# Kernel optimization log

Measured on AMD Instinct MI355X. Metric: run time of the kernel, lower is better.

The kernel has to match this reference:

```python
import math
import jax, jax.numpy as jnp
import numpy as np

H = 16
D_MODEL = 1024
D_K = D_MODEL // H


def setup_inputs() -> dict:
    key = jax.random.key(0)
    ks = jax.random.split(key, 12)
    B, S = 4, 2048
    scale = 1.0 / math.sqrt(D_MODEL)
    inp = {
        "query": jax.random.normal(ks[0], (B, S, D_MODEL), jnp.float32),
        "key": jax.random.normal(ks[1], (B, S, D_MODEL), jnp.float32),
        "value": jax.random.normal(ks[2], (B, S, D_MODEL), jnp.float32),
        "mask": jnp.ones((B, 1, 1, S), jnp.int32),
        "Wq": jax.random.normal(ks[3], (D_MODEL, D_MODEL), jnp.float32) * scale,
        "bq": jnp.zeros((D_MODEL,), jnp.float32),
        "Wk": jax.random.normal(ks[4], (D_MODEL, D_MODEL), jnp.float32) * scale,
        "bk": jnp.zeros((D_MODEL,), jnp.float32),
        "Wv": jax.random.normal(ks[5], (D_MODEL, D_MODEL), jnp.float32) * scale,
        "bv": jnp.zeros((D_MODEL,), jnp.float32),
        "Wo": jax.random.normal(ks[6], (D_MODEL, D_MODEL), jnp.float32) * scale,
        "bo": jnp.zeros((D_MODEL,), jnp.float32),
    }
    return inp


def _split_heads(x, W, b):
    # x: (B, S, d_model) -> (B, H, S, d_k); torch Linear: x @ W.T + b
    B, S, _ = x.shape
    y = x @ W.T + b
    return y.reshape(B, S, H, D_K).transpose(0, 2, 1, 3)


def reference(query, key, value, mask, Wq, bq, Wk, bk, Wv, bv, Wo, bo):
    B, Sq, _ = query.shape
    q = _split_heads(query, Wq, bq)   # (B,H,Sq,dk)
    k = _split_heads(key, Wk, bk)     # (B,H,Skv,dk)
    v = _split_heads(value, Wv, bv)   # (B,H,Skv,dk)
    scores = jnp.einsum('bhqd,bhkd->bhqk', q, k) / math.sqrt(D_K)
    scores = jnp.where(mask == 0, jnp.float32(-1e9), scores)
    p_attn = jax.nn.softmax(scores, axis=-1)  # dropout p=0 (eval)
    x = jnp.einsum('bhqk,bhkd->bhqd', p_attn, v)
    x = x.transpose(0, 2, 1, 3).reshape(B, Sq, H * D_K)
    return x @ Wo.T + bo
```

## Files before the change

### kernel.cpp

```cpp
#include <hip/hip_runtime.h>
#include <hip/hip_bf16.h>
#include <stdint.h>

typedef unsigned short u16;
typedef short bf16x8 __attribute__((ext_vector_type(8)));
typedef float f32x4 __attribute__((ext_vector_type(4)));

#define D_MODEL 1024
#define NHEAD 16
#define DK 64
#define SEQ 2048
#define NB 4
#define MTOT (NB * SEQ)

__device__ __forceinline__ u16 f2bf(float f) {
  union { float f; unsigned u; } x; x.f = f;
  unsigned r = x.u + 0x7FFFu + ((x.u >> 16) & 1u);
  return (u16)(r >> 16);
}
#if __has_builtin(__builtin_amdgcn_cvt_pk_bf16_f32)
__device__ __forceinline__ unsigned pkbf(float a, float b) {
  auto r = __builtin_amdgcn_cvt_pk_bf16_f32(a, b);
  union { decltype(r) v; unsigned u; } c; c.v = r; return c.u;
}
#else
__device__ __forceinline__ unsigned pkbf(float a, float b) {
  return (unsigned)f2bf(a) | ((unsigned)f2bf(b) << 16);
}
#endif
#if __has_builtin(__builtin_amdgcn_exp2f)
__device__ __forceinline__ float exp2r(float x) { return __builtin_amdgcn_exp2f(x); }
#else
__device__ __forceinline__ float exp2r(float x) { return exp2f(x); }
#endif
__device__ __forceinline__ void gl_lds16(const u16* g, u16* s) {
  __builtin_amdgcn_global_load_lds(
      (const __attribute__((address_space(1))) void*)g,
      (__attribute__((address_space(3))) void*)s, 16, 0, 0);
}

__global__ __launch_bounds__(256) void cvt1(const float4* __restrict__ src,
                                            uint2* __restrict__ dst, int n4) {
  for (int i = blockIdx.x * 256 + threadIdx.x; i < n4; i += gridDim.x * 256) {
    float4 x = src[i];
    uint2 o;
    o.x = pkbf(x.x, x.y);
    o.y = pkbf(x.z, x.w);
    dst[i] = o;
  }
}
__global__ __launch_bounds__(256) void cvt4(const float4* __restrict__ s0,
                                            const float4* __restrict__ s1,
                                            const float4* __restrict__ s2,
                                            const float4* __restrict__ s3,
                                            uint2* __restrict__ dst, int n4each) {
  const float4* s = (blockIdx.y == 0) ? s0 : (blockIdx.y == 1) ? s1
                  : (blockIdx.y == 2) ? s2 : s3;
  uint2* d = dst + (size_t)blockIdx.y * n4each;
  for (int i = blockIdx.x * 256 + threadIdx.x; i < n4each; i += gridDim.x * 256) {
    float4 x = s[i];
    uint2 o;
    o.x = pkbf(x.x, x.y);
    o.y = pkbf(x.z, x.w);
    d[i] = o;
  }
}

template <int MODE>
__global__ __launch_bounds__(256, 4) void gemm_bt64(
    const u16* __restrict__ A, const u16* __restrict__ W,
    const float* __restrict__ bias, void* __restrict__ out, float scale)
{
  __shared__ alignas(16) u16 smem[12288];
  u16* As = smem;
  u16* Bs = smem + 4096;

  const int tid = threadIdx.x;
  const int l = tid & 63, w = tid >> 6;
  const int lq = l & 15, qd = l >> 4;
  const int wm = (w >> 1) << 5, wn = (w & 1) << 6;
  const int m0 = blockIdx.y << 6, n0 = blockIdx.x << 7;

  int arow[2], ak8[2], brow[4], bk8[4];
#pragma unroll
  for (int r = 0; r < 2; ++r) {
    int c = r * 256 + tid;
    arow[r] = c >> 3; ak8[r] = (c & 7) ^ (arow[r] & 7);
  }
#pragma unroll
  for (int r = 0; r < 4; ++r) {
    int c = r * 256 + tid;
    brow[r] = c >> 3; bk8[r] = (c & 7) ^ (brow[r] & 7);
  }
  int aoff[2][2], boff[4][2];
#pragma unroll
  for (int i = 0; i < 2; ++i) {
    int mr = wm + (i << 4) + lq;
#pragma unroll
    for (int s = 0; s < 2; ++s)
      aoff[i][s] = (mr << 6) + ((((s << 2) + qd) ^ (mr & 7)) << 3);
  }
#pragma unroll
  for (int j = 0; j < 4; ++j) {
    int nr = wn + (j << 4) + lq;
#pragma unroll
    for (int s = 0; s < 2; ++s)
      boff[j][s] = (nr << 6) + ((((s << 2) + qd) ^ (nr & 7)) << 3);
  }

  const u16* Ab = A + (size_t)m0 * D_MODEL;
  const u16* Bb = W + (size_t)n0 * D_MODEL;

  f32x4 acc[2][4] = {};

  for (int kt = 0; kt < 16; ++kt) {
    const int kbase = kt << 6;
#pragma unroll
    for (int r = 0; r < 2; ++r)
      gl_lds16(Ab + (size_t)arow[r] * D_MODEL + kbase + (ak8[r] << 3), As + ((r * 256 + tid) << 3));
#pragma unroll
    for (int r = 0; r < 4; ++r)
      gl_lds16(Bb + (size_t)brow[r] * D_MODEL + kbase + (bk8[r] << 3), Bs + ((r * 256 + tid) << 3));
    __syncthreads();
#pragma unroll
    for (int s = 0; s < 2; ++s) {
      bf16x8 af[2], bfv[4];
#pragma unroll
      for (int i = 0; i < 2; ++i) af[i] = *(const bf16x8*)(As + aoff[i][s]);
#pragma unroll
      for (int j = 0; j < 4; ++j) bfv[j] = *(const bf16x8*)(Bs + boff[j][s]);
#pragma unroll
      for (int i = 0; i < 2; ++i)
#pragma unroll
        for (int j = 0; j < 4; ++j)
          acc[i][j] = __builtin_amdgcn_mfma_f32_16x16x32_bf16(af[i], bfv[j], acc[i][j], 0, 0, 0);
    }
    __syncthreads();
  }

  if (MODE == 1) {
    u16* Cs = smem;
    u16* outb = (u16*)out;
#pragma unroll
    for (int i = 0; i < 2; ++i)
#pragma unroll
      for (int j = 0; j < 4; ++j) {
        int ml = wm + (i << 4) + (qd << 2);
        int nl = wn + (j << 4) + lq;
        float bj = bias[n0 + nl];
        uint2 pk;
        pk.x = pkbf(acc[i][j][0] + bj, acc[i][j][1] + bj);
        pk.y = pkbf(acc[i][j][2] + bj, acc[i][j][3] + bj);
        *(uint2*)(Cs + nl * 80 + ml) = pk;
      }
    __syncthreads();
    int nl = tid >> 1, sh = (tid & 1) << 5;
    int n = n0 + nl;
    int b_ = m0 >> 11;
    const uint4* src = (const uint4*)(Cs + nl * 80 + sh);
    uint4* dst = (uint4*)(outb +
        (((size_t)b_ * NHEAD + (n >> 6)) * DK + (n & 63)) * SEQ + (m0 & 2047) + sh);
#pragma unroll
    for (int e = 0; e < 4; ++e) dst[e] = src[e];
  } else {
    u16* outb = (u16*)out;
    float* outf = (float*)out;
#pragma unroll
    for (int i = 0; i < 2; ++i)
#pragma unroll
      for (int j = 0; j < 4; ++j) {
        int ml = m0 + wm + (i << 4) + (qd << 2);
        int n = n0 + wn + (j << 4) + lq;
        float bj = bias[n];
#pragma unroll
        for (int r = 0; r < 4; ++r) {
          int m = ml + r;
          float v = (acc[i][j][r] + bj) * scale;
          if (MODE == 0)
            outb[(((size_t)(m >> 11) * NHEAD + (n >> 6)) * SEQ + (m & 2047)) * DK + (n & 63)] = f2bf(v);
          else
            outf[(size_t)m * D_MODEL + n] = v;
        }
      }
  }
}

__global__ __launch_bounds__(256, 4) void attn_fused(
    const u16* __restrict__ Q,
    const u16* __restrict__ K,
    const u16* __restrict__ Vt,
    const int* __restrict__ mask,
    u16* __restrict__ X)
{
  __shared__ alignas(16) u16 PQ[8192];
  __shared__ alignas(16) u16 Ks[4096];
  __shared__ alignas(16) u16 Vs[5120];
  __shared__ alignas(16) float mbf[64];

  const int tid = threadIdx.x;
  const int l = tid & 63, w = tid >> 6;
  const int lq = l & 15, qd = l >> 4;
  const int bh = blockIdx.y;
  const int q0 = blockIdx.x << 7;
  const int b_ = bh >> 4, h = bh & 15;
  const size_t base = (size_t)bh * SEQ * DK;
  const int wq0 = w << 5;

#pragma unroll
  for (int r = 0; r < 4; ++r) {
    int c = r * 256 + tid;
    int row = c >> 3, k8 = (c & 7) ^ (row & 7);
    gl_lds16(Q + base + (size_t)(q0 + row) * DK + (k8 << 3), PQ + (c << 3));
  }
  {
    unsigned v = (tid < 16) ? 0x3F803F80u : 0u;
    uint2 pk; pk.x = v; pk.y = v;
    *(uint2*)(Vs + 4096 + tid * 4) = pk;
  }
  __syncthreads();

  bf16x8 qf[2][2];
#pragma unroll
  for (int i = 0; i < 2; ++i)
#pragma unroll
    for (int s = 0; s < 2; ++s) {
      int row = wq0 + (i << 4) + lq;
      qf[i][s] = *(const bf16x8*)(PQ + (row << 6) + ((((s << 2) + qd) ^ (row & 7)) << 3));
    }

  f32x4 Ov[2][4] = {};
  f32x4 Ovl[2] = {};

  for (int t = 0; t < 32; ++t) {
    const int kv0 = t << 6;
    __syncthreads();
#pragma unroll
    for (int r = 0; r < 2; ++r) {
      int c = r * 256 + tid;
      int row = c >> 3, k8 = (c & 7) ^ (row & 7);
      gl_lds16(K + base + (size_t)(kv0 + row) * DK + (k8 << 3), Ks + (c << 3));
    }
#pragma unroll
    for (int r = 0; r < 2; ++r) {
      int c = r * 256 + tid;
      int row = c >> 3, k8 = (c & 7) ^ (row & 7);
      gl_lds16(Vt + base + (size_t)row * SEQ + kv0 + (k8 << 3), Vs + (c << 3));
    }
    if (tid < 64)
      mbf[tid] = mask[b_ * SEQ + kv0 + tid] ? 0.0f : -1.44269504e9f;
    __syncthreads();

    float4 m4[4];
#pragma unroll
    for (int jb = 0; jb < 4; ++jb) m4[jb] = *(const float4*)(mbf + (jb << 4) + (qd << 2));

    f32x4 Sc[4][2];
#pragma unroll
    for (int jb = 0; jb < 4; ++jb)
#pragma unroll
      for (int i = 0; i < 2; ++i) {
        Sc[jb][i][0] = m4[jb].x; Sc[jb][i][1] = m4[jb].y;
        Sc[jb][i][2] = m4[jb].z; Sc[jb][i][3] = m4[jb].w;
      }
#pragma unroll
    for (int s = 0; s < 2; ++s) {
      bf16x8 kf[4];
#pragma unroll
      for (int jb = 0; jb < 4; ++jb) {
        int row = (jb << 4) + lq;
        kf[jb] = *(const bf16x8*)(Ks + (row << 6) + ((((s << 2) + qd) ^ (row & 7)) << 3));
      }
#pragma unroll
      for (int jb = 0; jb < 4; ++jb)
#pragma unroll
        for (int i = 0; i < 2; ++i)
          Sc[jb][i] = __builtin_amdgcn_mfma_f32_16x16x32_bf16(kf[jb], qf[i][s], Sc[jb][i], 0, 0, 0);
    }

#pragma unroll
    for (int i = 0; i < 2; ++i) {
      const int prow = wq0 + (i << 4) + lq;
      const int rbase = prow << 6;
      const int rsw = prow & 7;
#pragma unroll
      for (int jb = 0; jb < 4; ++jb) {
        float p0 = exp2r(Sc[jb][i][0]);
        float p1 = exp2r(Sc[jb][i][1]);
        float p2 = exp2r(Sc[jb][i][2]);
        float p3 = exp2r(Sc[jb][i][3]);
        uint2 pk;
        pk.x = pkbf(p0, p1);
        pk.y = pkbf(p2, p3);
        int c = (jb << 1) + (qd >> 1);
        *(uint2*)(PQ + rbase + ((c ^ rsw) << 3) + ((qd & 1) << 2)) = pk;
      }
    }

#pragma unroll
    for (int s = 0; s < 2; ++s) {
      bf16x8 pf[2], vf[4], vf1;
#pragma unroll
      for (int i = 0; i < 2; ++i) {
        int prow = wq0 + (i << 4) + lq;
        pf[i] = *(const bf16x8*)(PQ + (prow << 6) + ((((s << 2) + qd) ^ (prow & 7)) << 3));
      }
#pragma unroll
      for (int j = 0; j < 4; ++j) {
        int row = (j << 4) + lq;
        vf[j] = *(const bf16x8*)(Vs + (row << 6) + ((((s << 2) + qd) ^ (row & 7)) << 3));
      }
      {
        int row = 64 + lq;
        vf1 = *(const bf16x8*)(Vs + (row << 6) + ((((s << 2) + qd) ^ (row & 7)) << 3));
      }
#pragma unroll
      for (int i = 0; i < 2; ++i) {
#pragma unroll
        for (int j = 0; j < 4; ++j)
          Ov[i][j] = __builtin_amdgcn_mfma_f32_16x16x32_bf16(pf[i], vf[j], Ov[i][j], 0, 0, 0);
        Ovl[i] = __builtin_amdgcn_mfma_f32_16x16x32_bf16(pf[i], vf1, Ovl[i], 0, 0, 0);
      }
    }
  }

#pragma unroll
  for (int i = 0; i < 2; ++i) {
    float inv[4];
#pragma unroll
    for (int r = 0; r < 4; ++r) inv[r] = 1.0f / Ovl[i][r];
#pragma unroll
    for (int r = 0; r < 4; ++r) {
      float sc_ = __shfl(inv[r], l & 48);
      int qrow = q0 + wq0 + (i << 4) + (qd << 2) + r;
#pragma unroll
      for (int j = 0; j < 4; ++j)
        X[((size_t)b_ * SEQ + qrow) * D_MODEL + (h << 6) + (j << 4) + lq] =
            f2bf(Ov[i][j][r] * sc_);
    }
  }
}

extern "C" void kernel_launch(void* const* d_in, const int* in_sizes, int n_in,
                              void* d_out, int out_size, void* d_ws, size_t ws_size,
                              hipStream_t stream) {
  const float* query = (const float*)d_in[0];
  const float* key_  = (const float*)d_in[1];
  const float* value = (const float*)d_in[2];
  const int* mask    = (const int*)d_in[3];
  const float* Wq = (const float*)d_in[4];
  const float* bq = (const float*)d_in[5];
  const float* Wk = (const float*)d_in[6];
  const float* bk = (const float*)d_in[7];
  const float* Wv = (const float*)d_in[8];
  const float* bv = (const float*)d_in[9];
  const float* Wo = (const float*)d_in[10];
  const float* bo = (const float*)d_in[11];

  u16* ws16 = (u16*)d_ws;
  const size_t WSZ = (size_t)D_MODEL * D_MODEL;
  const size_t ASZ = (size_t)MTOT * D_MODEL;
  u16* wqc = ws16;
  u16* wkc = ws16 + WSZ;
  u16* wvc = ws16 + 2 * WSZ;
  u16* woc = ws16 + 3 * WSZ;
  u16* C1  = ws16 + 4 * WSZ;
  u16* Qb  = ws16 + 4 * WSZ + ASZ;
  u16* Kb  = ws16 + 4 * WSZ + 2 * ASZ;
  u16* Xb  = C1;
  u16* Vtb = (u16*)d_out;

  const float SCQ = 0.125f * 1.44269504088896f;

  dim3 blk(256);
  dim3 gg(D_MODEL / 128, MTOT / 64);

  cvt4<<<dim3(256, 4), blk, 0, stream>>>((const float4*)Wq, (const float4*)Wk,
                                         (const float4*)Wv, (const float4*)Wo,
                                         (uint2*)wqc, (int)(WSZ / 4));
  cvt1<<<1024, blk, 0, stream>>>((const float4*)query, (uint2*)C1, (int)(ASZ / 4));
  gemm_bt64<0><<<gg, blk, 0, stream>>>(C1, wqc, bq, Qb, SCQ);
  cvt1<<<1024, blk, 0, stream>>>((const float4*)key_, (uint2*)C1, (int)(ASZ / 4));
  gemm_bt64<0><<<gg, blk, 0, stream>>>(C1, wkc, bk, Kb, 1.0f);
  cvt1<<<1024, blk, 0, stream>>>((const float4*)value, (uint2*)C1, (int)(ASZ / 4));
  gemm_bt64<1><<<gg, blk, 0, stream>>>(C1, wvc, bv, Vtb, 1.0f);
  attn_fused<<<dim3(SEQ / 128, NB * NHEAD), blk, 0, stream>>>(Qb, Kb, Vtb, mask, Xb);
  gemm_bt64<2><<<gg, blk, 0, stream>>>(Xb, woc, bo, d_out, 1.0f);
}
```

Measured before the change: 363.7 us.

## Batch all fp32-to-bf16 conversions and QKV projections into single launches

Result: faster. 349.6 us (-3.9%).

```diff
diff --git a/kernel.cpp b/kernel.cpp
--- a/kernel.cpp
+++ b/kernel.cpp
@@ -39,6 +39,24 @@
       (__attribute__((address_space(3))) void*)s, 16, 0, 0);
 }
 
+struct CvtArgs {
+  const float4* s[7];
+  uint2* d[7];
+  int n4[7];
+};
+__global__ __launch_bounds__(256) void cvt_all(CvtArgs a) {
+  const int y = blockIdx.y;
+  const float4* s = a.s[y];
+  uint2* d = a.d[y];
+  const int n4 = a.n4[y];
+  for (int i = blockIdx.x * 256 + threadIdx.x; i < n4; i += gridDim.x * 256) {
+    float4 x = s[i];
+    uint2 o;
+    o.x = pkbf(x.x, x.y);
+    o.y = pkbf(x.z, x.w);
+    d[i] = o;
+  }
+}
 __global__ __launch_bounds__(256) void cvt1(const float4* __restrict__ src,
                                             uint2* __restrict__ dst, int n4) {
   for (int i = blockIdx.x * 256 + threadIdx.x; i < n4; i += gridDim.x * 256) {
@@ -67,11 +85,11 @@
 }
 
 template <int MODE>
-__global__ __launch_bounds__(256, 4) void gemm_bt64(
+__device__ __forceinline__ void gemm_body(
     const u16* __restrict__ A, const u16* __restrict__ W,
-    const float* __restrict__ bias, void* __restrict__ out, float scale)
+    const float* __restrict__ bias, void* __restrict__ out, float scale,
+    int m0, int n0, u16* smem)
 {
-  __shared__ alignas(16) u16 smem[12288];
   u16* As = smem;
   u16* Bs = smem + 4096;
 
@@ -79,7 +97,6 @@
   const int l = tid & 63, w = tid >> 6;
   const int lq = l & 15, qd = l >> 4;
   const int wm = (w >> 1) << 5, wn = (w & 1) << 6;
-  const int m0 = blockIdx.y << 6, n0 = blockIdx.x << 7;
 
   int arow[2], ak8[2], brow[4], bk8[4];
 #pragma unroll
@@ -183,6 +200,33 @@
         }
       }
   }
+}
+
+template <int MODE>
+__global__ __launch_bounds__(256, 4) void gemm_bt64(
+    const u16* __restrict__ A, const u16* __restrict__ W,
+    const float* __restrict__ bias, void* __restrict__ out, float scale)
+{
+  __shared__ alignas(16) u16 smem[12288];
+  gemm_body<MODE>(A, W, bias, out, scale,
+                  blockIdx.y << 6, blockIdx.x << 7, smem);
+}
+
+__global__ __launch_bounds__(256, 4) void proj_qkv(
+    const u16* __restrict__ Cq, const u16* __restrict__ Ck, const u16* __restrict__ Cv,
+    const u16* __restrict__ wq, const u16* __restrict__ wk, const u16* __restrict__ wv,
+    const float* __restrict__ bq, const float* __restrict__ bk, const float* __restrict__ bv,
+    u16* __restrict__ Qb, u16* __restrict__ Kb, u16* __restrict__ Vt, float scq)
+{
+  __shared__ alignas(16) u16 smem[12288];
+  const int z = blockIdx.z;
+  const int m0 = blockIdx.y << 6, n0 = blockIdx.x << 7;
+  if (z == 0)
+    gemm_body<0>(Cq, wq, bq, Qb, scq, m0, n0, smem);
+  else if (z == 1)
+    gemm_body<0>(Ck, wk, bk, Kb, 1.0f, m0, n0, smem);
+  else
+    gemm_body<1>(Cv, wv, bv, Vt, 1.0f, m0, n0, smem);
 }
 
 __global__ __launch_bounds__(256, 4) void attn_fused(
@@ -359,30 +403,59 @@
   u16* ws16 = (u16*)d_ws;
   const size_t WSZ = (size_t)D_MODEL * D_MODEL;
   const size_t ASZ = (size_t)MTOT * D_MODEL;
-  u16* wqc = ws16;
-  u16* wkc = ws16 + WSZ;
-  u16* wvc = ws16 + 2 * WSZ;
-  u16* woc = ws16 + 3 * WSZ;
-  u16* C1  = ws16 + 4 * WSZ;
-  u16* Qb  = ws16 + 4 * WSZ + ASZ;
-  u16* Kb  = ws16 + 4 * WSZ + 2 * ASZ;
-  u16* Xb  = C1;
-  u16* Vtb = (u16*)d_out;
-
   const float SCQ = 0.125f * 1.44269504088896f;
 
   dim3 blk(256);
   dim3 gg(D_MODEL / 128, MTOT / 64);
 
-  cvt4<<<dim3(256, 4), blk, 0, stream>>>((const float4*)Wq, (const float4*)Wk,
-                                         (const float4*)Wv, (const float4*)Wo,
-                                         (uint2*)wqc, (int)(WSZ / 4));
-  cvt1<<<1024, blk, 0, stream>>>((const float4*)query, (uint2*)C1, (int)(ASZ / 4));
-  gemm_bt64<0><<<gg, blk, 0, stream>>>(C1, wqc, bq, Qb, SCQ);
-  cvt1<<<1024, blk, 0, stream>>>((const float4*)key_, (uint2*)C1, (int)(ASZ / 4));
-  gemm_bt64<0><<<gg, blk, 0, stream>>>(C1, wkc, bk, Kb, 1.0f);
-  cvt1<<<1024, blk, 0, stream>>>((const float4*)value, (uint2*)C1, (int)(ASZ / 4));
-  gemm_bt64<1><<<gg, blk, 0, stream>>>(C1, wvc, bv, Vtb, 1.0f);
-  attn_fused<<<dim3(SEQ / 128, NB * NHEAD), blk, 0, stream>>>(Qb, Kb, Vtb, mask, Xb);
-  gemm_bt64<2><<<gg, blk, 0, stream>>>(Xb, woc, bo, d_out, 1.0f);
-}
+  if (ws_size >= (size_t)(4 * WSZ + 4 * ASZ) * 2) {
+    u16* wqc = ws16;
+    u16* wkc = ws16 + WSZ;
+    u16* wvc = ws16 + 2 * WSZ;
+    u16* woc = ws16 + 3 * WSZ;
+    u16* Cq  = ws16 + 4 * WSZ;
+    u16* Ck  = ws16 + 4 * WSZ + ASZ;
+    u16* Qb  = ws16 + 4 * WSZ + 2 * ASZ;
+    u16* Kb  = ws16 + 4 * WSZ + 3 * ASZ;
+    u16* Xb  = Cq;
+    u16* Vtb = (u16*)d_out;
+    u16* Cv  = (u16*)d_out + ASZ;
+
+    CvtArgs ca;
+    ca.s[0] = (const float4*)query; ca.d[0] = (uint2*)Cq;  ca.n4[0] = (int)(ASZ / 4);
+    ca.s[1] = (const float4*)key_;  ca.d[1] = (uint2*)Ck;  ca.n4[1] = (int)(ASZ / 4);
+    ca.s[2] = (const float4*)value; ca.d[2] = (uint2*)Cv;  ca.n4[2] = (int)(ASZ / 4);
+    ca.s[3] = (const float4*)Wq;    ca.d[3] = (uint2*)wqc; ca.n4[3] = (int)(WSZ / 4);
+    ca.s[4] = (const float4*)Wk;    ca.d[4] = (uint2*)wkc; ca.n4[4] = (int)(WSZ / 4);
+    ca.s[5] = (const float4*)Wv;    ca.d[5] = (uint2*)wvc; ca.n4[5] = (int)(WSZ / 4);
+    ca.s[6] = (const float4*)Wo;    ca.d[6] = (uint2*)woc; ca.n4[6] = (int)(WSZ / 4);
+
+    cvt_all<<<dim3(512, 7), blk, 0, stream>>>(ca);
+    proj_qkv<<<dim3(D_MODEL / 128, MTOT / 64, 3), blk, 0, stream>>>(
+        Cq, Ck, Cv, wqc, wkc, wvc, bq, bk, bv, Qb, Kb, Vtb, SCQ);
+    attn_fused<<<dim3(SEQ / 128, NB * NHEAD), blk, 0, stream>>>(Qb, Kb, Vtb, mask, Xb);
+    gemm_bt64<2><<<gg, blk, 0, stream>>>(Xb, woc, bo, d_out, 1.0f);
+  } else {
+    u16* wqc = ws16;
+    u16* wkc = ws16 + WSZ;
+    u16* wvc = ws16 + 2 * WSZ;
+    u16* woc = ws16 + 3 * WSZ;
+    u16* C1  = ws16 + 4 * WSZ;
+    u16* Qb  = ws16 + 4 * WSZ + ASZ;
+    u16* Kb  = ws16 + 4 * WSZ + 2 * ASZ;
+    u16* Xb  = C1;
+    u16* Vtb = (u16*)d_out;
+
+    cvt4<<<dim3(256, 4), blk, 0, stream>>>((const float4*)Wq, (const float4*)Wk,
+                                           (const float4*)Wv, (const float4*)Wo,
+                                           (uint2*)wqc, (int)(WSZ / 4));
+    cvt1<<<1024, blk, 0, stream>>>((const float4*)query, (uint2*)C1, (int)(ASZ / 4));
+    gemm_bt64<0><<<gg, blk, 0, stream>>>(C1, wqc, bq, Qb, SCQ);
+    cvt1<<<1024, blk, 0, stream>>>((const float4*)key_, (uint2*)C1, (int)(ASZ / 4));
+    gemm_bt64<0><<<gg, blk, 0, stream>>>(C1, wkc, bk, Kb, 1.0f);
+    cvt1<<<1024, blk, 0, stream>>>((const float4*)value, (uint2*)C1, (int)(ASZ / 4));
+    gemm_bt64<1><<<gg, blk, 0, stream>>>(C1, wvc, bv, Vtb, 1.0f);
+    attn_fused<<<dim3(SEQ / 128, NB * NHEAD), blk, 0, stream>>>(Qb, Kb, Vtb, mask, Xb);
+    gemm_bt64<2><<<gg, blk, 0, stream>>>(Xb, woc, bo, d_out, 1.0f);
+  }
+}
```
